# Optimization experiments

Measured on AMD Instinct MI355X. Metric: run time of the kernel, lower is better.

## Reference

```python
import jax, jax.numpy as jnp
import numpy as np

B, S, D = 1, 2048, 6144
H, KV, HD = 48, 8, 128  # query heads, kv heads, head dim
THETA = 10000.0


def _rope_tables(seq_len, head_dim, theta):
    pos = jnp.arange(seq_len, dtype=jnp.float32)
    inv_freq = 1.0 / (theta ** (jnp.arange(0, head_dim, 2, dtype=jnp.float32) / head_dim))
    freqs = pos[:, None] * inv_freq[None, :]                 # [S, HD/2]
    emb = jnp.concatenate([freqs, freqs], axis=-1)           # [S, HD]
    return jnp.cos(emb), jnp.sin(emb)


def setup_inputs() -> dict:
    key = jax.random.key(0)
    k1, k2, k3 = jax.random.split(key, 3)
    hidden_states = jax.random.normal(k1, (B, S, D), dtype=jnp.float32) * 0.02
    w_qkv = jax.random.normal(k2, (D, (H + 2 * KV) * HD), dtype=jnp.float32) * 0.02
    w_out = jax.random.normal(k3, (H * HD, D), dtype=jnp.float32) * 0.02
    cos, sin = _rope_tables(S, HD, THETA)
    return {"hidden_states": hidden_states, "cos": cos, "sin": sin,
            "w_qkv": w_qkv, "w_out": w_out}


def _rotate_half(x):
    x1, x2 = jnp.split(x, 2, axis=-1)
    return jnp.concatenate([-x2, x1], axis=-1)


def reference(hidden_states, cos, sin, w_qkv, w_out):
    b, s, d = hidden_states.shape
    # fused QKV projection
    qkv = jnp.einsum('bsd,de->bse', hidden_states, w_qkv)
    q = qkv[..., : H * HD].reshape(b, s, H, HD)
    k = qkv[..., H * HD: (H + KV) * HD].reshape(b, s, KV, HD)
    v = qkv[..., (H + KV) * HD:].reshape(b, s, KV, HD)
    # rotary embedding (rotate-half form)
    c = cos[None, :, None, :]
    sn = sin[None, :, None, :]
    q = q * c + _rotate_half(q) * sn
    k = k * c + _rotate_half(k) * sn
    # GQA: expand kv heads to query heads
    rep = H // KV
    k = jnp.repeat(k, rep, axis=2)  # [b, s, H, HD]
    v = jnp.repeat(v, rep, axis=2)
    scale = 1.0 / jnp.sqrt(jnp.float32(HD))
    scores = jnp.einsum('bqhd,bkhd->bhqk', q, k) * scale     # [b,H,S,S]
    causal = jnp.tril(jnp.ones((s, s), dtype=bool))
    scores = jnp.where(causal[None, None], scores, jnp.float32(-1e30))
    attn = jax.nn.softmax(scores, axis=-1)
    out = jnp.einsum('bhqk,bkhd->bqhd', attn, v).reshape(b, s, H * HD)
    return jnp.einsum('bsd,de->bse', out, w_out)
```

## Files before the change

kernel.cpp:

```cpp
#include <hip/hip_runtime.h>


#define S_   2048
#define D_   6144
#define H_   48
#define KV_  8
#define HD_  128
#define NQK  8192
#define REP  6

typedef __attribute__((ext_vector_type(8)))  __bf16 bf16x8;
typedef __attribute__((ext_vector_type(4)))  __bf16 bf16x4;
typedef __attribute__((ext_vector_type(2)))  __bf16 bf16x2;
typedef __attribute__((ext_vector_type(4)))  float  f32x4;
typedef __attribute__((ext_vector_type(16))) float  f32x16;
typedef __attribute__((ext_vector_type(4)))  float  float4v;

__device__ __forceinline__ void gl_lds16(const void* g, void* l) {
  __builtin_amdgcn_global_load_lds(
      (const __attribute__((address_space(1))) void*)g,
      (__attribute__((address_space(3))) void*)l, 16, 0, 0);
}

__device__ __forceinline__ unsigned pack2(float a, float b) {
  union { bf16x2 v; unsigned u; } x;
  x.v[0] = (__bf16)a; x.v[1] = (__bf16)b;
  return x.u;
}

__global__ __launch_bounds__(256) void cvt_bf16(const float* __restrict__ in,
                                                __bf16* __restrict__ out, int n4) {
  int stride = gridDim.x * 256;
  for (int i = blockIdx.x * 256 + threadIdx.x; i < n4; i += stride) {
    float4v v = ((const float4v*)in)[i];
    bf16x4 o;
    o[0] = (__bf16)v[0]; o[1] = (__bf16)v[1];
    o[2] = (__bf16)v[2]; o[3] = (__bf16)v[3];
    ((bf16x4*)out)[i] = o;
  }
}

__global__ __launch_bounds__(256) void wtrans(const float* __restrict__ src,
                                              __bf16* __restrict__ dst,
                                              int K, int N) {
  __shared__ float t[32][33];
  const int n0 = blockIdx.x * 32, k0 = blockIdx.y * 32;
  const int tx = threadIdx.x, ty = threadIdx.y;
#pragma unroll
  for (int r = 0; r < 4; ++r)
    t[ty + r * 8][tx] = src[(size_t)(k0 + ty + r * 8) * N + n0 + tx];
  __syncthreads();
#pragma unroll
  for (int r = 0; r < 4; ++r)
    dst[(size_t)(n0 + ty + r * 8) * K + k0 + tx] = (__bf16)t[tx][ty + r * 8];
}

template <typename CT, int BN>
__global__ __launch_bounds__(512, 2) void gemm_bt(const __bf16* __restrict__ A,
                                                  const __bf16* __restrict__ BT,
                                                  CT* __restrict__ C,
                                                  int M, int N, int K) {
  constexpr int NB = BN / 64;
  constexpr int NF = BN / 64;
  __shared__ __align__(16) __bf16 As[2][256 * 64];
  __shared__ __align__(16) __bf16 Bs[2][BN * 64];
  const int tid = threadIdx.x;
  const int w = tid >> 6, l = tid & 63;
  const int lr = l & 15, lg = l >> 4;
  const int wm = w >> 2, wn = w & 3;
  const int nwg = gridDim.x * gridDim.y;
  int bid = blockIdx.y * gridDim.x + blockIdx.x;
  bid = (bid & 7) * (nwg >> 3) + (bid >> 3);
  const int m0 = (bid / gridDim.x) * 256, n0 = (bid % gridDim.x) * BN;
  const int nkt = K >> 6;

  auto stage_all = [&](int T) {
    const int buf = T & 1, k0 = T << 6;
#pragma unroll
    for (int j = 0; j < 4; ++j) {
      int idx = j * 512 + tid;
      int row = idx >> 3;
      int c = (idx & 7) ^ (row & 7);
      gl_lds16(A + (size_t)(m0 + row) * K + k0 + c * 8,
               As[buf] + (size_t)(j * 512 + w * 64) * 8);
    }
#pragma unroll
    for (int j = 0; j < NB; ++j) {
      int idx = j * 512 + tid;
      int row = idx >> 3;
      int c = (idx & 7) ^ (row & 7);
      gl_lds16(BT + (size_t)(n0 + row) * K + k0 + c * 8,
               Bs[buf] + (size_t)(j * 512 + w * 64) * 8);
    }
  };
  auto rdA = [&](const __bf16* Ab, int mh, int kk, bf16x8* afr) {
#pragma unroll
    for (int m = 0; m < 4; ++m) {
      int row = wm * 128 + (mh * 4 + m) * 16 + lr;
      afr[m] = *(const bf16x8*)(Ab + (size_t)row * 64
                                + (((kk * 4 + lg) ^ (lr & 7)) * 8));
    }
  };
  auto rdB = [&](const __bf16* Bb, int kk, bf16x8* bfr) {
#pragma unroll
    for (int n = 0; n < NF; ++n) {
      int row = wn * (BN / 4) + n * 16 + lr;
      bfr[n] = *(const bf16x8*)(Bb + (size_t)row * 64
                                + (((kk * 4 + lg) ^ (lr & 7)) * 8));
    }
  };
#define SBAR  __builtin_amdgcn_s_barrier()
#define MFMA_CLUSTER(ACC_OFF)                                                   \
  __builtin_amdgcn_s_setprio(1);                                               \
  _Pragma("unroll")                                                             \
  for (int m = 0; m < 4; ++m)                                                   \
    _Pragma("unroll")                                                           \
    for (int n = 0; n < NF; ++n)                                                \
      acc[(ACC_OFF) + m][n] = __builtin_amdgcn_mfma_f32_16x16x32_bf16(          \
          afr[m], bfr[n], acc[(ACC_OFF) + m][n], 0, 0, 0);                      \
  __builtin_amdgcn_s_setprio(0)

  f32x4 acc[8][NF] = {};
  stage_all(0);
  asm volatile("s_waitcnt vmcnt(0)" ::: "memory");
  SBAR;

  for (int T = 0; T < nkt; ++T) {
    const __bf16* Ab = As[T & 1];
    const __bf16* Bb = Bs[T & 1];
    bf16x8 afr[4], bfr[NF];
    rdA(Ab, 0, 0, afr);
    rdB(Bb, 0, bfr);
    if (T + 1 < nkt) stage_all(T + 1);
    MFMA_CLUSTER(0);
    SBAR;
    rdA(Ab, 1, 0, afr);
    MFMA_CLUSTER(4);
    SBAR;
    rdA(Ab, 0, 1, afr);
    rdB(Bb, 1, bfr);
    MFMA_CLUSTER(0);
    SBAR;
    rdA(Ab, 1, 1, afr);
    MFMA_CLUSTER(4);
    asm volatile("s_waitcnt lgkmcnt(0)" ::: "memory");
    if (T + 1 < nkt) asm volatile("s_waitcnt vmcnt(0)" ::: "memory");
    SBAR;
  }
#undef SBAR
#undef MFMA_CLUSTER
#pragma unroll
  for (int m = 0; m < 8; ++m)
#pragma unroll
    for (int n = 0; n < NF; ++n)
#pragma unroll
      for (int j = 0; j < 4; ++j) {
        int row = m0 + wm * 128 + m * 16 + lg * 4 + j;
        int col = n0 + wn * (BN / 4) + n * 16 + lr;
        C[(size_t)row * N + col] = (CT)acc[m][n][j];
      }
}

__global__ __launch_bounds__(256) void rope_qk(const __bf16* __restrict__ qkv,
                                               const float* __restrict__ cosT,
                                               const float* __restrict__ sinT,
                                               __bf16* __restrict__ Qo,
                                               __bf16* __restrict__ Ko) {
  const int s = blockIdx.x;
  const __bf16* base = qkv + (size_t)s * NQK;
  const float* ct = cosT + s * HD_;
  const float* st = sinT + s * HD_;
  const float scale = 0.1275174313f;
  for (int q4 = threadIdx.x; q4 < H_ * HD_ / 4; q4 += 256) {
    int h = q4 >> 5, d = (q4 & 31) * 4;
    bf16x4 x  = *(const bf16x4*)(base + h * HD_ + d);
    bf16x4 xr = (d < 64) ? *(const bf16x4*)(base + h * HD_ + d + 64)
                         : *(const bf16x4*)(base + h * HD_ + d - 64);
    float4v c4 = *(const float4v*)(ct + d);
    float4v s4 = *(const float4v*)(st + d);
    bf16x4 o;
#pragma unroll
    for (int j = 0; j < 4; ++j) {
      float r = (d < 64) ? -(float)xr[j] : (float)xr[j];
      o[j] = (__bf16)(((float)x[j] * c4[j] + r * s4[j]) * scale);
    }
    *(bf16x4*)(Qo + ((size_t)s * H_ + h) * HD_ + d) = o;
  }
  for (int q4 = threadIdx.x; q4 < KV_ * HD_ / 4; q4 += 256) {
    int h = q4 >> 5, d = (q4 & 31) * 4;
    const __bf16* kb = base + H_ * HD_;
    bf16x4 x  = *(const bf16x4*)(kb + h * HD_ + d);
    bf16x4 xr = (d < 64) ? *(const bf16x4*)(kb + h * HD_ + d + 64)
                         : *(const bf16x4*)(kb + h * HD_ + d - 64);
    float4v c4 = *(const float4v*)(ct + d);
    float4v s4 = *(const float4v*)(st + d);
    bf16x4 o;
#pragma unroll
    for (int j = 0; j < 4; ++j) {
      float r = (d < 64) ? -(float)xr[j] : (float)xr[j];
      o[j] = (__bf16)((float)x[j] * c4[j] + r * s4[j]);
    }
    *(bf16x4*)(Ko + ((size_t)s * KV_ + h) * HD_ + d) = o;
  }
}

__global__ __launch_bounds__(256) void v_trans(const __bf16* __restrict__ qkv,
                                               __bf16* __restrict__ Vt) {
  __shared__ __bf16 t[32][36];
  const int s0 = blockIdx.x * 32, d0 = blockIdx.y * 32, h = blockIdx.z;
  const int tx = threadIdx.x, ty = threadIdx.y;
  *(bf16x4*)&t[ty][tx * 4] =
      *(const bf16x4*)(qkv + (size_t)(s0 + ty) * NQK + (H_ + KV_) * HD_ + h * HD_ + d0 + tx * 4);
  __syncthreads();
  bf16x4 o;
#pragma unroll
  for (int j = 0; j < 4; ++j) o[j] = t[tx * 4 + j][ty];
  *(bf16x4*)(Vt + ((size_t)h * HD_ + d0 + ty) * S_ + s0 + tx * 4) = o;
}

__global__ __launch_bounds__(256, 2) void attn(const __bf16* __restrict__ Q,
                                               const __bf16* __restrict__ Kb,
                                               const __bf16* __restrict__ Vt,
                                               __bf16* __restrict__ O) {
  __shared__ __align__(16) __bf16 Ks[2][64 * 128];
  __shared__ __align__(16) __bf16 Vs[2][128 * 64];
  const int bx = blockIdx.x, h = blockIdx.y, kvh = h / REP;
  const int tid = threadIdx.x, w = tid >> 6, l = tid & 63;
  const int c = l & 31, g = l >> 5;
  const int qb = bx * 128;
  const int qrow = qb + w * 32 + c;
  const int tmax_w = (qb + w * 32 + 31) >> 6;
  const int NT = (qb >> 6) + 2;

  auto stage = [&](int t) {
    const int buf = t & 1;
    const int kbase = t << 6;
#pragma unroll
    for (int j = 0; j < 4; ++j) {
      int idx = j * 256 + tid;
      int row = idx >> 4, cc = (idx & 15) ^ (row & 15);
      gl_lds16(Kb + ((size_t)(kbase + row) * KV_ + kvh) * HD_ + cc * 8,
               Ks[buf] + (size_t)(j * 256 + w * 64) * 8);
    }
#pragma unroll
    for (int j = 0; j < 4; ++j) {
      int idx = j * 256 + tid;
      int row = idx >> 3, cc = (idx & 7) ^ (row & 7);
      gl_lds16(Vt + (size_t)(kvh * HD_ + row) * S_ + kbase + cc * 8,
               Vs[buf] + (size_t)(j * 256 + w * 64) * 8);
    }
  };

  bf16x8 qf[8];
  const __bf16* qp = Q + ((size_t)qrow * H_ + h) * HD_ + g * 8;
#pragma unroll
  for (int st = 0; st < 8; ++st) qf[st] = *(const bf16x8*)(qp + st * 16);

  f32x16 o[4] = {};
  float m = -1e30f, lsum = 0.f;

  stage(0);
  __syncthreads();
  for (int t = 0; t < NT; ++t) {
    const int buf = t & 1;
    if (t + 1 < NT) stage(t + 1);
    if (t <= tmax_w) {
      const int kbase = t << 6;
      f32x16 s0 = {}, s1 = {};
      __builtin_amdgcn_s_setprio(1);
#pragma unroll
      for (int st = 0; st < 8; ++st) {
        int ch = ((st * 2 + g) ^ (c & 15)) * 8;
        bf16x8 k0 = *(const bf16x8*)(Ks[buf] + (size_t)c * 128 + ch);
        bf16x8 k1 = *(const bf16x8*)(Ks[buf] + (size_t)(32 + c) * 128 + ch);
        s0 = __builtin_amdgcn_mfma_f32_32x32x16_bf16(k0, qf[st], s0, 0, 0, 0);
        s1 = __builtin_amdgcn_mfma_f32_32x32x16_bf16(k1, qf[st], s1, 0, 0, 0);
      }
      __builtin_amdgcn_s_setprio(0);
      if (t == tmax_w) {
#pragma unroll
        for (int r = 0; r < 16; ++r) {
          int krow = (r & 3) + 8 * (r >> 2) + 4 * g;
          if (kbase + krow > qrow)      s0[r] = -1e30f;
          if (kbase + 32 + krow > qrow) s1[r] = -1e30f;
        }
      }
      float mj = s0[0];
#pragma unroll
      for (int r = 1; r < 16; ++r) mj = fmaxf(mj, s0[r]);
#pragma unroll
      for (int r = 0; r < 16; ++r) mj = fmaxf(mj, s1[r]);
      mj = fmaxf(mj, __shfl_xor(mj, 32));
      float mnew = fmaxf(m, mj);
      float sc = __builtin_amdgcn_exp2f(m - mnew);
      float rs = 0.f;
      float p0[16], p1[16];
#pragma unroll
      for (int r = 0; r < 16; ++r) { p0[r] = __builtin_amdgcn_exp2f(s0[r] - mnew); rs += p0[r]; }
#pragma unroll
      for (int r = 0; r < 16; ++r) { p1[r] = __builtin_amdgcn_exp2f(s1[r] - mnew); rs += p1[r]; }
      rs += __shfl_xor(rs, 32);
      lsum = lsum * sc + rs;
      m = mnew;
#pragma unroll
      for (int db = 0; db < 4; ++db)
#pragma unroll
        for (int r = 0; r < 16; ++r) o[db][r] *= sc;
      unsigned bq[4][4];
#pragma unroll
      for (int n = 0; n < 2; ++n)
#pragma unroll
        for (int tq = 0; tq < 2; ++tq) {
          const float* pp = n ? p1 : p0;
          unsigned q0 = pack2(pp[8 * tq + 0], pp[8 * tq + 1]);
          unsigned q1 = pack2(pp[8 * tq + 2], pp[8 * tq + 3]);
          unsigned q2 = pack2(pp[8 * tq + 4], pp[8 * tq + 5]);
          unsigned q3 = pack2(pp[8 * tq + 6], pp[8 * tq + 7]);
          unsigned v0 = g ? q0 : q2;
          unsigned v1 = g ? q1 : q3;
          unsigned sh0 = (unsigned)__shfl_xor((int)v0, 32);
          unsigned sh1 = (unsigned)__shfl_xor((int)v1, 32);
          int s = n * 2 + tq;
          bq[s][0] = g ? sh0 : q0;
          bq[s][1] = g ? sh1 : q1;
          bq[s][2] = g ? q2 : sh0;
          bq[s][3] = g ? q3 : sh1;
        }
      __builtin_amdgcn_s_setprio(1);
#pragma unroll
      for (int s = 0; s < 4; ++s) {
        union { unsigned u[4]; bf16x8 v; } bb;
        bb.u[0] = bq[s][0]; bb.u[1] = bq[s][1]; bb.u[2] = bq[s][2]; bb.u[3] = bq[s][3];
#pragma unroll
        for (int db = 0; db < 4; ++db) {
          int ch = ((s * 2 + g) ^ (c & 7)) * 8;
          bf16x8 vfr = *(const bf16x8*)(Vs[buf] + (size_t)(db * 32 + c) * 64 + ch);
          o[db] = __builtin_amdgcn_mfma_f32_32x32x16_bf16(vfr, bb.v, o[db], 0, 0, 0);
        }
      }
      __builtin_amdgcn_s_setprio(0);
    }
    if (t + 1 < NT) __syncthreads();
  }
  float inv = 1.f / lsum;
#pragma unroll
  for (int db = 0; db < 4; ++db)
#pragma unroll
    for (int rg = 0; rg < 4; ++rg) {
      bf16x4 ov;
#pragma unroll
      for (int j = 0; j < 4; ++j) ov[j] = (__bf16)(o[db][rg * 4 + j] * inv);
      *(bf16x4*)(O + (size_t)qrow * D_ + h * HD_ + db * 32 + rg * 8 + g * 4) = ov;
    }
}

extern "C" void kernel_launch(void* const* d_in, const int* in_sizes, int n_in,
                              void* d_out, int out_size, void* d_ws, size_t ws_size,
                              hipStream_t stream) {
  const float* hidden = (const float*)d_in[0];
  const float* cosT   = (const float*)d_in[1];
  const float* sinT   = (const float*)d_in[2];
  const float* w_qkv  = (const float*)d_in[3];
  const float* w_out  = (const float*)d_in[4];
  float* out = (float*)d_out;
  char* ws = (char*)d_ws;

  __bf16* wT   = (__bf16*)ws;
  __bf16* hb   = (__bf16*)(ws + 100663296);
  __bf16* qkvb = (__bf16*)(ws + 100663296 + 25165824);
  __bf16* q_b  = (__bf16*)(ws + 100663296 + 25165824 + 33554432);
  __bf16* k_b  = q_b + (size_t)S_ * H_ * HD_;
  __bf16* vt_b = k_b + (size_t)S_ * KV_ * HD_;

  cvt_bf16<<<dim3(2048), dim3(256), 0, stream>>>(hidden, hb, (int)((size_t)S_ * D_ / 4));
  wtrans<<<dim3(NQK / 32, D_ / 32), dim3(32, 8), 0, stream>>>(w_qkv, wT, D_, NQK);
  gemm_bt<__bf16, 256><<<dim3(NQK / 256, S_ / 256), dim3(512), 0, stream>>>(hb, wT, qkvb, S_, NQK, D_);
  rope_qk<<<dim3(S_), dim3(256), 0, stream>>>(qkvb, cosT, sinT, q_b, k_b);
  v_trans<<<dim3(S_ / 32, HD_ / 32, KV_), dim3(8, 32), 0, stream>>>(qkvb, vt_b);
  wtrans<<<dim3(D_ / 32, D_ / 32), dim3(32, 8), 0, stream>>>(w_out, wT, D_, D_);
  attn<<<dim3(S_ / 128, H_), dim3(256), 0, stream>>>(q_b, k_b, vt_b, hb);
  gemm_bt<float, 192><<<dim3(D_ / 192, S_ / 256), dim3(512), 0, stream>>>(hb, wT, out, S_, D_, D_);
}
```

Baseline: 662.2 us.

## Add 128x128 output-projection GEMM, reverse attention block order, lazy softmax rescale

The output projection now uses a new 128x128-tile GEMM with 256 threads, two blocks per CU and an XCD-aware block remap, in place of the 256x192 tile. The aim is more workgroups and better CU fill on the 2048x6144 output. The attention kernel walks query blocks in reverse order so the long causal blocks start first. Its online softmax skips rescaling the running max and the O accumulator unless the max grows by more than 8 in log2 units, trading a small risk of larger exponentials for fewer multiplies per tile.

```diff
diff --git a/kernel.cpp b/kernel.cpp
--- a/kernel.cpp
+++ b/kernel.cpp
@@ -161,6 +161,90 @@
       }
 }
 
+template <typename CT>
+__global__ __launch_bounds__(256, 2) void gemm_bt128(const __bf16* __restrict__ A,
+                                                     const __bf16* __restrict__ BT,
+                                                     CT* __restrict__ C,
+                                                     int M, int N, int K) {
+  __shared__ __align__(16) __bf16 As[2][128 * 64];
+  __shared__ __align__(16) __bf16 Bs[2][128 * 64];
+  const int tid = threadIdx.x;
+  const int w = tid >> 6, l = tid & 63;
+  const int lr = l & 15, lg = l >> 4;
+  const int wm = w >> 1, wn = w & 1;
+  const int nwg = gridDim.x * gridDim.y;
+  int bid = blockIdx.y * gridDim.x + blockIdx.x;
+  bid = (bid & 7) * (nwg >> 3) + (bid >> 3);
+  const int m0 = (bid / gridDim.x) * 128, n0 = (bid % gridDim.x) * 128;
+  const int nkt = K >> 6;
+
+  auto stage_all = [&](int T) {
+    const int buf = T & 1, k0 = T << 6;
+#pragma unroll
+    for (int j = 0; j < 4; ++j) {
+      int idx = j * 256 + tid;
+      int row = idx >> 3;
+      int c = (idx & 7) ^ (row & 7);
+      gl_lds16(A + (size_t)(m0 + row) * K + k0 + c * 8,
+               As[buf] + (size_t)(j * 256 + w * 64) * 8);
+      gl_lds16(BT + (size_t)(n0 + row) * K + k0 + c * 8,
+               Bs[buf] + (size_t)(j * 256 + w * 64) * 8);
+    }
+  };
+  auto rd = [&](const __bf16* Sb, int rbase, int kk, bf16x8* fr) {
+#pragma unroll
+    for (int m = 0; m < 4; ++m) {
+      int row = rbase + m * 16 + lr;
+      fr[m] = *(const bf16x8*)(Sb + (size_t)row * 64
+                               + (((kk * 4 + lg) ^ (lr & 7)) * 8));
+    }
+  };
+
+  f32x4 acc[4][4] = {};
+  stage_all(0);
+  asm volatile("s_waitcnt vmcnt(0)" ::: "memory");
+  __builtin_amdgcn_s_barrier();
+
+  for (int T = 0; T < nkt; ++T) {
+    const __bf16* Ab = As[T & 1];
+    const __bf16* Bb = Bs[T & 1];
+    bf16x8 afr[4], bfr[4];
+    rd(Ab, wm * 64, 0, afr);
+    rd(Bb, wn * 64, 0, bfr);
+    if (T + 1 < nkt) stage_all(T + 1);
+    __builtin_amdgcn_s_setprio(1);
+#pragma unroll
+    for (int m = 0; m < 4; ++m)
+#pragma unroll
+      for (int n = 0; n < 4; ++n)
+        acc[m][n] = __builtin_amdgcn_mfma_f32_16x16x32_bf16(afr[m], bfr[n], acc[m][n], 0, 0, 0);
+    __builtin_amdgcn_s_setprio(0);
+    __builtin_amdgcn_s_barrier();
+    rd(Ab, wm * 64, 1, afr);
+    rd(Bb, wn * 64, 1, bfr);
+    __builtin_amdgcn_s_setprio(1);
+#pragma unroll
+    for (int m = 0; m < 4; ++m)
+#pragma unroll
+      for (int n = 0; n < 4; ++n)
+        acc[m][n] = __builtin_amdgcn_mfma_f32_16x16x32_bf16(afr[m], bfr[n], acc[m][n], 0, 0, 0);
+    __builtin_amdgcn_s_setprio(0);
+    asm volatile("s_waitcnt lgkmcnt(0)" ::: "memory");
+    if (T + 1 < nkt) asm volatile("s_waitcnt vmcnt(0)" ::: "memory");
+    __builtin_amdgcn_s_barrier();
+  }
+#pragma unroll
+  for (int m = 0; m < 4; ++m)
+#pragma unroll
+    for (int n = 0; n < 4; ++n)
+#pragma unroll
+      for (int j = 0; j < 4; ++j) {
+        int row = m0 + wm * 64 + m * 16 + lg * 4 + j;
+        int col = n0 + wn * 64 + n * 16 + lr;
+        C[(size_t)row * N + col] = (CT)acc[m][n][j];
+      }
+}
+
 __global__ __launch_bounds__(256) void rope_qk(const __bf16* __restrict__ qkv,
                                                const float* __restrict__ cosT,
                                                const float* __restrict__ sinT,
@@ -224,7 +308,8 @@
                                                __bf16* __restrict__ O) {
   __shared__ __align__(16) __bf16 Ks[2][64 * 128];
   __shared__ __align__(16) __bf16 Vs[2][128 * 64];
-  const int bx = blockIdx.x, h = blockIdx.y, kvh = h / REP;
+  const int bx = gridDim.x - 1 - blockIdx.x;
+  const int h = blockIdx.y, kvh = h / REP;
   const int tid = threadIdx.x, w = tid >> 6, l = tid & 63;
   const int c = l & 31, g = l >> 5;
   const int qb = bx * 128;
@@ -291,21 +376,24 @@
 #pragma unroll
       for (int r = 0; r < 16; ++r) mj = fmaxf(mj, s1[r]);
       mj = fmaxf(mj, __shfl_xor(mj, 32));
-      float mnew = fmaxf(m, mj);
-      float sc = __builtin_amdgcn_exp2f(m - mnew);
+      if (!__all(mj - m <= 8.0f)) {
+        float mnew = fmaxf(m, mj);
+        float sc = __builtin_amdgcn_exp2f(m - mnew);
+        lsum *= sc;
+#pragma unroll
+        for (int db = 0; db < 4; ++db)
+#pragma unroll
+          for (int r = 0; r < 16; ++r) o[db][r] *= sc;
+        m = mnew;
+      }
       float rs = 0.f;
       float p0[16], p1[16];
 #pragma unroll
-      for (int r = 0; r < 16; ++r) { p0[r] = __builtin_amdgcn_exp2f(s0[r] - mnew); rs += p0[r]; }
-#pragma unroll
-      for (int r = 0; r < 16; ++r) { p1[r] = __builtin_amdgcn_exp2f(s1[r] - mnew); rs += p1[r]; }
+      for (int r = 0; r < 16; ++r) { p0[r] = __builtin_amdgcn_exp2f(s0[r] - m); rs += p0[r]; }
+#pragma unroll
+      for (int r = 0; r < 16; ++r) { p1[r] = __builtin_amdgcn_exp2f(s1[r] - m); rs += p1[r]; }
       rs += __shfl_xor(rs, 32);
-      lsum = lsum * sc + rs;
-      m = mnew;
-#pragma unroll
-      for (int db = 0; db < 4; ++db)
-#pragma unroll
-        for (int r = 0; r < 16; ++r) o[db][r] *= sc;
+      lsum += rs;
       unsigned bq[4][4];
 #pragma unroll
       for (int n = 0; n < 2; ++n)
@@ -379,5 +467,5 @@
   v_trans<<<dim3(S_ / 32, HD_ / 32, KV_), dim3(8, 32), 0, stream>>>(qkvb, vt_b);
   wtrans<<<dim3(D_ / 32, D_ / 32), dim3(32, 8), 0, stream>>>(w_out, wT, D_, D_);
   attn<<<dim3(S_ / 128, H_), dim3(256), 0, stream>>>(q_b, k_b, vt_b, hb);
-  gemm_bt<float, 192><<<dim3(D_ / 192, S_ / 256), dim3(512), 0, stream>>>(hb, wT, out, S_, D_, D_);
-}
+  gemm_bt128<float><<<dim3(D_ / 128, S_ / 128), dim3(256), 0, stream>>>(hb, wT, out, S_, D_, D_);
+}
```

Result: slower. 678.7 us (+2.5%).
